# Kernel tuning notes

Hardware: AMD Instinct MI355X
Metric: run time of the kernel (lower is better)

## Reference

```python
import jax, jax.numpy as jnp
import numpy as np


def setup_inputs() -> dict:
    key = jax.random.key(0)
    k1, k2 = jax.random.split(key)
    B, N, M, D = 4, 8192, 8192, 3
    pc1 = jax.random.normal(k1, (B, N, D), dtype=jnp.float32)
    pc2 = jax.random.normal(k2, (B, M, D), dtype=jnp.float32)
    return {"pc1": pc1, "pc2": pc2}


def _chamfer_one(a, b):
    # a: [N, 3], b: [M, 3]
    # squared pairwise distances via ||a||^2 + ||b||^2 - 2 a.b (avoids [N,M,3] intermediate)
    a2 = jnp.sum(a * a, axis=-1)          # [N]
    b2 = jnp.sum(b * b, axis=-1)          # [M]
    d2 = a2[:, None] + b2[None, :] - 2.0 * jnp.einsum('nd,md->nm', a, b)  # [N, M]
    d2 = jnp.maximum(d2, 0.0)
    # bidirectional nearest-neighbor min-reduction, averaged per direction
    return jnp.mean(jnp.min(d2, axis=1)) + jnp.mean(jnp.min(d2, axis=0))


def reference(pc1, pc2):
    # transpose_mode=False: points already [N, d]. Per-batch scalar chamfer distance.
    D = jax.vmap(_chamfer_one)(pc1.astype(jnp.float32), pc2.astype(jnp.float32))  # [B]
    return jnp.squeeze(D)
```

## Files before the change

kernel.cpp:

```cpp
#include <hip/hip_runtime.h>
#include <hip/hip_fp16.h>
#include <math.h>


#define BATCH   4
#define NPTS    8192
#define THREADS 256
#define NCHUNKS 32
#define MSLICES 8
#define MSL     1024
#define SC      256.0f
#define ISC     (1.0f/256.0f)
#define FLT_BIG 3.4e38f

typedef _Float16 half8 __attribute__((ext_vector_type(8)));
typedef float f32x16 __attribute__((ext_vector_type(16)));

union U4H8 { uint4 u; half8 h; };

__device__ __forceinline__ unsigned pk(__half lo, __half hi) {
    return (unsigned)__half_as_ushort(lo) | ((unsigned)__half_as_ushort(hi) << 16);
}
__device__ __forceinline__ unsigned enc_f32(float f) {
    unsigned b = __float_as_uint(f);
    return (b & 0x80000000u) ? ~b : (b | 0x80000000u);
}
__device__ __forceinline__ float dec_f32(unsigned k) {
    unsigned b = (k & 0x80000000u) ? (k & 0x7FFFFFFFu) : ~k;
    return __uint_as_float(b);
}

__global__ __launch_bounds__(THREADS) void chamfer_mfma_kernel(
        const float* __restrict__ pc1, const float* __restrict__ pc2,
        float* __restrict__ part_row, float* __restrict__ part_col,
        float* __restrict__ out) {
    const int bid    = blockIdx.x;
    const int mslice = bid & 7;
    const int nchunk = (bid >> 3) & 31;
    const int batch  = bid >> 8;

    if (bid == 0 && threadIdx.x < BATCH) out[threadIdx.x] = 0.0f;

    __shared__ unsigned smem[9472];
    unsigned* colmin = &smem[8448];

    const int t = threadIdx.x;
    const int L = t & 63;
    const int w = t >> 6;
    const int g = L >> 5;
    const __half one = __float2half(1.0f);
    const __half z0  = __float2half(0.0f);

    const float* bb = pc2 + ((size_t)batch * NPTS + (size_t)mslice * MSL) * 3;
    #pragma unroll
    for (int k = 0; k < 4; ++k) {
        const int p = k * THREADS + t;
        const float x = bb[3 * p + 0], y = bb[3 * p + 1], z = bb[3 * p + 2];
        __half hx = __float2half(x), hy = __float2half(y), hz = __float2half(z);
        __half lx = __float2half((x - __half2float(hx)) * SC);
        __half ly = __float2half((y - __half2float(hy)) * SC);
        __half lz = __float2half((z - __half2float(hz)) * SC);
        __half sx = __float2half(__half2float(hx) * ISC);
        __half sy = __float2half(__half2float(hy) * ISC);
        __half sz = __float2half(__half2float(hz) * ISC);
        const float b2 = fmaf(x, x, fmaf(y, y, z * z));
        __half hb2 = __float2half(b2);
        __half lb2 = __float2half(b2 - __half2float(hb2));
        uint4* g0 = (uint4*)&smem[p * 4];
        uint4* g1 = (uint4*)&smem[4096 + p * 4];
        *g0 = make_uint4(pk(hx, hy), pk(hz, sx), pk(sy, sz), pk(one, hb2));
        *g1 = make_uint4(pk(lx, ly), pk(lz, one), pk(lb2, z0), pk(z0, z0));
    }
    #pragma unroll
    for (int i = 0; i < 4; ++i) colmin[i * THREADS + t] = 0xFFFFFFFFu;

    U4H8 A[2];
    #pragma unroll
    for (int ti = 0; ti < 2; ++ti) {
        const int n = nchunk * 256 + w * 64 + (L & 31) + ti * 32;
        const float* ap = pc1 + ((size_t)batch * NPTS + n) * 3;
        const float x = ap[0], y = ap[1], z = ap[2];
        const float vx = -2.0f * x, vy = -2.0f * y, vz = -2.0f * z;
        __half Hx = __float2half(vx), Hy = __float2half(vy), Hz = __float2half(vz);
        __half Lx = __float2half((vx - __half2float(Hx)) * SC);
        __half Ly = __float2half((vy - __half2float(Hy)) * SC);
        __half Lz = __float2half((vz - __half2float(Hz)) * SC);
        __half Sx = __float2half(__half2float(Hx) * ISC);
        __half Sy = __float2half(__half2float(Hy) * ISC);
        __half Sz = __float2half(__half2float(Hz) * ISC);
        const float a2 = fmaf(x, x, fmaf(y, y, z * z));
        __half ha2 = __float2half(a2);
        __half la2 = __float2half(a2 - __half2float(ha2));
        if (g == 0) {
            A[ti].u = make_uint4(pk(Hx, Hy), pk(Hz, Lx), pk(Ly, Lz), pk(ha2, one));
        } else {
            A[ti].u = make_uint4(pk(Sx, Sy), pk(Sz, la2), pk(one, z0), pk(z0, z0));
        }
    }

    __syncthreads();

    const f32x16 zf = {0.0f};
    float rm0[16], rm1[16];
    #pragma unroll
    for (int r = 0; r < 16; ++r) { rm0[r] = FLT_BIG; rm1[r] = FLT_BIG; }

    const int rbase = g * 4096 + (L & 31) * 4;
    for (int mt = 0; mt < 32; mt += 2) {
        U4H8 b0, b1;
        b0.u = *(const uint4*)&smem[rbase + mt * 128];
        b1.u = *(const uint4*)&smem[rbase + mt * 128 + 128];
        f32x16 d0a = __builtin_amdgcn_mfma_f32_32x32x16_f16(A[0].h, b0.h, zf, 0, 0, 0);
        f32x16 d1a = __builtin_amdgcn_mfma_f32_32x32x16_f16(A[1].h, b0.h, zf, 0, 0, 0);
        f32x16 d0b = __builtin_amdgcn_mfma_f32_32x32x16_f16(A[0].h, b1.h, zf, 0, 0, 0);
        f32x16 d1b = __builtin_amdgcn_mfma_f32_32x32x16_f16(A[1].h, b1.h, zf, 0, 0, 0);
        float c0 = FLT_BIG, c1 = FLT_BIG;
        #pragma unroll
        for (int r = 0; r < 16; ++r) {
            rm0[r] = fminf(fminf(rm0[r], d0a[r]), d0b[r]);
            rm1[r] = fminf(fminf(rm1[r], d1a[r]), d1b[r]);
            c0 = fminf(fminf(c0, d0a[r]), d1a[r]);
            c1 = fminf(fminf(c1, d0b[r]), d1b[r]);
        }
        c0 = fminf(c0, __shfl_xor(c0, 32, 64));
        c1 = fminf(c1, __shfl_xor(c1, 32, 64));
        const float cv = (L < 32) ? c0 : c1;
        atomicMin(&colmin[mt * 32 + L], enc_f32(cv));
    }

    __syncthreads();
    float* sf = (float*)smem;
    const int wbase = w * 2112;
    #pragma unroll
    for (int r = 0; r < 16; ++r) {
        const int row0 = (r & 3) + 8 * (r >> 2) + 4 * g;
        sf[wbase + row0 * 33 + (L & 31)] = rm0[r];
        sf[wbase + (row0 + 32) * 33 + (L & 31)] = rm1[r];
    }
    __syncthreads();

    float v = FLT_BIG;
    const int rb = wbase + L * 33;
    #pragma unroll
    for (int i = 0; i < 32; ++i) v = fminf(v, sf[rb + i]);
    const int grow = nchunk * 256 + w * 64 + L;
    part_row[((size_t)batch * MSLICES + mslice) * NPTS + grow] = v;

    #pragma unroll
    for (int i = 0; i < 4; ++i) {
        const int j = i * THREADS + t;
        part_col[((size_t)batch * NCHUNKS + nchunk) * NPTS + mslice * MSL + j] =
            dec_f32(colmin[j]);
    }
}

__global__ __launch_bounds__(THREADS) void chamfer_reduce_kernel(
        const float* __restrict__ part_row, const float* __restrict__ part_col,
        float* __restrict__ out) {
    const int idx   = blockIdx.x * THREADS + threadIdx.x;
    const int dir   = idx >> 15;
    const int batch = (idx >> 13) & 3;
    const int n     = idx & (NPTS - 1);

    float v = FLT_BIG;
    if (dir == 0) {
        const float* pb = part_row + (size_t)batch * MSLICES * NPTS + n;
        #pragma unroll
        for (int s = 0; s < MSLICES; ++s) v = fminf(v, pb[(size_t)s * NPTS]);
    } else {
        const float* pb = part_col + (size_t)batch * NCHUNKS * NPTS + n;
        #pragma unroll
        for (int s = 0; s < NCHUNKS; ++s) v = fminf(v, pb[(size_t)s * NPTS]);
    }
    float d2 = fmaxf(v, 0.0f);

    #pragma unroll
    for (int off = 32; off > 0; off >>= 1)
        d2 += __shfl_down(d2, off, 64);

    __shared__ float wsum[THREADS / 64];
    if ((threadIdx.x & 63) == 0) wsum[threadIdx.x >> 6] = d2;
    __syncthreads();

    if (threadIdx.x == 0) {
        float ssum = 0.0f;
        #pragma unroll
        for (int wv = 0; wv < THREADS / 64; ++wv) ssum += wsum[wv];
        atomicAdd(&out[batch], ssum * (1.0f / (float)NPTS));
    }
}

extern "C" void kernel_launch(void* const* d_in, const int* in_sizes, int n_in,
                              void* d_out, int out_size, void* d_ws, size_t ws_size,
                              hipStream_t stream) {
    const float* pc1 = (const float*)d_in[0];
    const float* pc2 = (const float*)d_in[1];
    float* out      = (float*)d_out;
    float* part_row = (float*)d_ws;
    float* part_col = part_row + (size_t)BATCH * MSLICES * NPTS;

    chamfer_mfma_kernel<<<BATCH * NCHUNKS * MSLICES, THREADS, 0, stream>>>(
        pc1, pc2, part_row, part_col, out);
    chamfer_reduce_kernel<<<(2 * BATCH * NPTS) / THREADS, THREADS, 0, stream>>>(
        part_row, part_col, out);
}
```

Baseline: 79.18 us.

## Split M into 16 slices, halve LDS, and raise occupancy with launch bounds

The pc2 axis is cut into 16 slices of 512 points instead of 8 of 1024. This doubles the grid to 2048 blocks and halves the shared memory per block. Launch bounds now ask for 5 blocks per SIMD-level occupancy. The inner loop handles one B tile per iteration, and the row-min staging is redone per wave in two halves, so each block needs one fewer barrier. In exchange, the reduce kernel must read twice as many row partials, and each block repeats the A-fragment setup over a smaller amount of work.

```diff
diff --git a/kernel.cpp b/kernel.cpp
--- a/kernel.cpp
+++ b/kernel.cpp
@@ -7,8 +7,8 @@
 #define NPTS    8192
 #define THREADS 256
 #define NCHUNKS 32
-#define MSLICES 8
-#define MSL     1024
+#define MSLICES 16
+#define MSL     512
 #define SC      256.0f
 #define ISC     (1.0f/256.0f)
 #define FLT_BIG 3.4e38f
@@ -30,19 +30,19 @@
     return __uint_as_float(b);
 }
 
-__global__ __launch_bounds__(THREADS) void chamfer_mfma_kernel(
+__global__ __launch_bounds__(THREADS, 5) void chamfer_mfma_kernel(
         const float* __restrict__ pc1, const float* __restrict__ pc2,
         float* __restrict__ part_row, float* __restrict__ part_col,
         float* __restrict__ out) {
     const int bid    = blockIdx.x;
-    const int mslice = bid & 7;
-    const int nchunk = (bid >> 3) & 31;
-    const int batch  = bid >> 8;
+    const int mslice = bid & 15;
+    const int nchunk = (bid >> 4) & 31;
+    const int batch  = bid >> 9;
 
     if (bid == 0 && threadIdx.x < BATCH) out[threadIdx.x] = 0.0f;
 
-    __shared__ unsigned smem[9472];
-    unsigned* colmin = &smem[8448];
+    __shared__ unsigned smem[4736];
+    unsigned* colmin = &smem[4224];
 
     const int t = threadIdx.x;
     const int L = t & 63;
@@ -53,7 +53,7 @@
 
     const float* bb = pc2 + ((size_t)batch * NPTS + (size_t)mslice * MSL) * 3;
     #pragma unroll
-    for (int k = 0; k < 4; ++k) {
+    for (int k = 0; k < 2; ++k) {
         const int p = k * THREADS + t;
         const float x = bb[3 * p + 0], y = bb[3 * p + 1], z = bb[3 * p + 2];
         __half hx = __float2half(x), hy = __float2half(y), hz = __float2half(z);
@@ -67,12 +67,12 @@
         __half hb2 = __float2half(b2);
         __half lb2 = __float2half(b2 - __half2float(hb2));
         uint4* g0 = (uint4*)&smem[p * 4];
-        uint4* g1 = (uint4*)&smem[4096 + p * 4];
+        uint4* g1 = (uint4*)&smem[2048 + p * 4];
         *g0 = make_uint4(pk(hx, hy), pk(hz, sx), pk(sy, sz), pk(one, hb2));
         *g1 = make_uint4(pk(lx, ly), pk(lz, one), pk(lb2, z0), pk(z0, z0));
     }
-    #pragma unroll
-    for (int i = 0; i < 4; ++i) colmin[i * THREADS + t] = 0xFFFFFFFFu;
+    colmin[t] = 0xFFFFFFFFu;
+    colmin[THREADS + t] = 0xFFFFFFFFu;
 
     U4H8 A[2];
     #pragma unroll
@@ -105,52 +105,62 @@
     #pragma unroll
     for (int r = 0; r < 16; ++r) { rm0[r] = FLT_BIG; rm1[r] = FLT_BIG; }
 
-    const int rbase = g * 4096 + (L & 31) * 4;
-    for (int mt = 0; mt < 32; mt += 2) {
-        U4H8 b0, b1;
-        b0.u = *(const uint4*)&smem[rbase + mt * 128];
-        b1.u = *(const uint4*)&smem[rbase + mt * 128 + 128];
-        f32x16 d0a = __builtin_amdgcn_mfma_f32_32x32x16_f16(A[0].h, b0.h, zf, 0, 0, 0);
-        f32x16 d1a = __builtin_amdgcn_mfma_f32_32x32x16_f16(A[1].h, b0.h, zf, 0, 0, 0);
-        f32x16 d0b = __builtin_amdgcn_mfma_f32_32x32x16_f16(A[0].h, b1.h, zf, 0, 0, 0);
-        f32x16 d1b = __builtin_amdgcn_mfma_f32_32x32x16_f16(A[1].h, b1.h, zf, 0, 0, 0);
-        float c0 = FLT_BIG, c1 = FLT_BIG;
+    const int rbase = g * 2048 + (L & 31) * 4;
+    for (int mt = 0; mt < 16; ++mt) {
+        U4H8 b;
+        b.u = *(const uint4*)&smem[rbase + mt * 128];
+        f32x16 d0 = __builtin_amdgcn_mfma_f32_32x32x16_f16(A[0].h, b.h, zf, 0, 0, 0);
+        f32x16 d1 = __builtin_amdgcn_mfma_f32_32x32x16_f16(A[1].h, b.h, zf, 0, 0, 0);
+        float c = FLT_BIG;
         #pragma unroll
         for (int r = 0; r < 16; ++r) {
-            rm0[r] = fminf(fminf(rm0[r], d0a[r]), d0b[r]);
-            rm1[r] = fminf(fminf(rm1[r], d1a[r]), d1b[r]);
-            c0 = fminf(fminf(c0, d0a[r]), d1a[r]);
-            c1 = fminf(fminf(c1, d0b[r]), d1b[r]);
+            rm0[r] = fminf(rm0[r], d0[r]);
+            rm1[r] = fminf(rm1[r], d1[r]);
+            c = fminf(fminf(c, d0[r]), d1[r]);
         }
-        c0 = fminf(c0, __shfl_xor(c0, 32, 64));
-        c1 = fminf(c1, __shfl_xor(c1, 32, 64));
-        const float cv = (L < 32) ? c0 : c1;
-        atomicMin(&colmin[mt * 32 + L], enc_f32(cv));
+        c = fminf(c, __shfl_xor(c, 32, 64));
+        if (L < 32) atomicMin(&colmin[mt * 32 + L], enc_f32(c));
     }
 
     __syncthreads();
+
+    #pragma unroll
+    for (int i = 0; i < 2; ++i) {
+        const int j = i * THREADS + t;
+        part_col[((size_t)batch * NCHUNKS + nchunk) * NPTS + mslice * MSL + j] =
+            dec_f32(colmin[j]);
+    }
+
     float* sf = (float*)smem;
-    const int wbase = w * 2112;
+    const int wbase = w * 1056;
+    const int row = L & 31, ch = L >> 5;
+    const size_t prow_base = ((size_t)batch * MSLICES + mslice) * NPTS
+                           + nchunk * 256 + w * 64;
     #pragma unroll
     for (int r = 0; r < 16; ++r) {
         const int row0 = (r & 3) + 8 * (r >> 2) + 4 * g;
         sf[wbase + row0 * 33 + (L & 31)] = rm0[r];
-        sf[wbase + (row0 + 32) * 33 + (L & 31)] = rm1[r];
-    }
-    __syncthreads();
-
-    float v = FLT_BIG;
-    const int rb = wbase + L * 33;
-    #pragma unroll
-    for (int i = 0; i < 32; ++i) v = fminf(v, sf[rb + i]);
-    const int grow = nchunk * 256 + w * 64 + L;
-    part_row[((size_t)batch * MSLICES + mslice) * NPTS + grow] = v;
-
-    #pragma unroll
-    for (int i = 0; i < 4; ++i) {
-        const int j = i * THREADS + t;
-        part_col[((size_t)batch * NCHUNKS + nchunk) * NPTS + mslice * MSL + j] =
-            dec_f32(colmin[j]);
+    }
+    {
+        const float* rp = &sf[wbase + row * 33 + ch * 16];
+        float v = rp[0];
+        #pragma unroll
+        for (int i = 1; i < 16; ++i) v = fminf(v, rp[i]);
+        v = fminf(v, __shfl_xor(v, 32, 64));
+        if (L < 32) part_row[prow_base + row] = v;
+    }
+    #pragma unroll
+    for (int r = 0; r < 16; ++r) {
+        const int row0 = (r & 3) + 8 * (r >> 2) + 4 * g;
+        sf[wbase + row0 * 33 + (L & 31)] = rm1[r];
+    }
+    {
+        const float* rp = &sf[wbase + row * 33 + ch * 16];
+        float v = rp[0];
+        #pragma unroll
+        for (int i = 1; i < 16; ++i) v = fminf(v, rp[i]);
+        v = fminf(v, __shfl_xor(v, 32, 64));
+        if (L < 32) part_row[prow_base + 32 + row] = v;
     }
 }
 
```

After: 95.05 us. +20.0%, slower.
